# Performance work log

Measured on AMD Instinct MI355X. Metric: run time of the kernel, lower is better.

The kernel has to match this reference:

```python
import jax, jax.numpy as jnp
import numpy as np

D = 512
H = 8
DV = D // H  # 64
NEG_INF = -1e30


def setup_inputs() -> dict:
    key = jax.random.key(0)
    ks = jax.random.split(key, 10)
    B, S = 4, 2048
    x = jax.random.normal(ks[0], (B, D, S), dtype=jnp.float32)
    mask = jnp.ones((B, S), dtype=jnp.float32)
    s = 1.0 / np.sqrt(D)
    sv = 1.0 / np.sqrt(D)
    # per-head Linear(d -> dv) weights stacked: [H, dv, d] (torch Linear layout W @ x)
    Wq = jax.random.uniform(ks[1], (H, DV, D), jnp.float32, -s, s)
    bq = jax.random.uniform(ks[2], (H, DV), jnp.float32, -s, s)
    Wk = jax.random.uniform(ks[3], (H, DV, D), jnp.float32, -s, s)
    bk = jax.random.uniform(ks[4], (H, DV), jnp.float32, -s, s)
    Wv = jax.random.uniform(ks[5], (H, DV, D), jnp.float32, -s, s)
    bv = jax.random.uniform(ks[6], (H, DV), jnp.float32, -s, s)
    W0 = jax.random.uniform(ks[7], (D, D), jnp.float32, -sv, sv)
    b0 = jax.random.uniform(ks[8], (D,), jnp.float32, -sv, sv)
    return {"x": x, "mask": mask, "Wq": Wq, "bq": bq, "Wk": Wk, "bk": bk,
            "Wv": Wv, "bv": bv, "W0": W0, "b0": b0}


def reference(x, mask, Wq, bq, Wk, bk, Wv, bv, W0, b0):
    # x: [B, d, S] -> xt: [B, S, d]
    xt = jnp.transpose(x, (0, 2, 1))
    # fused per-head projections: [B, H, S, dv]
    q = jnp.einsum('bsd,hed->bhse', xt, Wq) + bq[None, :, None, :]
    k = jnp.einsum('bsd,hed->bhse', xt, Wk) + bk[None, :, None, :]
    v = jnp.einsum('bsd,hed->bhse', xt, Wv) + bv[None, :, None, :]
    dv = q.shape[-1]
    scores = jnp.einsum('bhse,bhte->bhst', q, k) * (1.0 / np.sqrt(dv))
    # mask_logits (QANet style): keep where mask==1, else -1e30; mask over key dim
    h_mask = mask[:, None, None, :]  # [B,1,1,S]
    scores = scores * h_mask + (1.0 - h_mask) * NEG_INF
    p = jax.nn.softmax(scores, axis=-1)
    # zero out fully-masked query rows via v_mask on query dim
    p = p * mask[:, None, :, None]
    out = jnp.einsum('bhst,bhte->bhse', p, v)  # [B,H,S,dv]
    # concat heads along feature dim -> [B, S, d]
    B, _, S, _ = out.shape
    heads = jnp.transpose(out, (0, 2, 1, 3)).reshape(B, S, -1)
    y = heads @ W0.T + b0  # output projection
    return jnp.transpose(y, (0, 2, 1))  # [B, d, S]
```

## Files before the change

kernel.cpp:

```cpp
#include <hip/hip_runtime.h>

#define B_  4
#define D_  512
#define H_  8
#define DV_ 64
#define S_  2048
#define LDT 72

typedef __bf16 bf16;
typedef bf16  bf16x8 __attribute__((ext_vector_type(8)));
typedef bf16  bf16x4 __attribute__((ext_vector_type(4)));
typedef float f32x4  __attribute__((ext_vector_type(4)));

#define MFMA(a, b, c) __builtin_amdgcn_mfma_f32_16x16x32_bf16((a), (b), (c), 0, 0, 0)

__global__ __launch_bounds__(256) void transpose_x(const float* __restrict__ x,
                                                   bf16* __restrict__ xb) {
    __shared__ float tile[32][33];
    const int bidx = blockIdx.x;
    const int sblk = bidx % (S_ / 32);
    const int dblk = (bidx / (S_ / 32)) % (D_ / 32);
    const int b    = bidx / ((S_ / 32) * (D_ / 32));
    const int d0 = dblk * 32, s0 = sblk * 32;
    const int tx = threadIdx.x & 31;
    const int ty = threadIdx.x >> 5;
    const float* xp = x + (size_t)b * D_ * S_;
#pragma unroll
    for (int i = 0; i < 32; i += 8)
        tile[ty + i][tx] = xp[(size_t)(d0 + ty + i) * S_ + s0 + tx];
    __syncthreads();
    bf16* xbp = xb + ((size_t)b * S_ + s0) * D_ + d0;
#pragma unroll
    for (int i = 0; i < 32; i += 8)
        xbp[(size_t)(ty + i) * D_ + tx] = (bf16)tile[tx][ty + i];
}

__global__ __launch_bounds__(256) void gemm_qkv(
    const bf16* __restrict__ A,
    const float* __restrict__ Wq, const float* __restrict__ Wk, const float* __restrict__ Wv,
    const float* __restrict__ bq, const float* __restrict__ bk, const float* __restrict__ bv,
    bf16* __restrict__ Q, bf16* __restrict__ K, bf16* __restrict__ Vt) {
    __shared__ bf16 As[128][LDT];
    __shared__ bf16 Bs[64][LDT];

    const int tid  = threadIdx.x;
    const int w    = tid >> 6, lane = tid & 63;
    const int m16  = lane & 15, quad = lane >> 4;

    const int nblk = blockIdx.x % 24;
    const int mblk = blockIdx.x / 24;
    const int m0 = mblk * 128;
    const int n0 = nblk * 64;
    const int proj = n0 >> 9;
    const int nr   = n0 & 511;
    const float* W    = (proj == 0) ? Wq : (proj == 1) ? Wk : Wv;
    const float* bias = (proj == 0) ? bq : (proj == 1) ? bk : bv;

    f32x4 acc[2][4];
#pragma unroll
    for (int i = 0; i < 2; ++i)
#pragma unroll
        for (int j = 0; j < 4; ++j) acc[i][j] = (f32x4){0.f, 0.f, 0.f, 0.f};

    for (int k0 = 0; k0 < D_; k0 += 64) {
        __syncthreads();
        {
            const int col = (tid & 7) * 8;
            const int row = tid >> 3;
#pragma unroll
            for (int p = 0; p < 4; ++p) {
                const int r = row + p * 32;
                *(bf16x8*)&As[r][col] = *(const bf16x8*)&A[(size_t)(m0 + r) * D_ + k0 + col];
            }
        }
        {
            const int col = (tid & 15) * 4;
            const int row = tid >> 4;
#pragma unroll
            for (int p = 0; p < 4; ++p) {
                const int r = row + p * 16;
                const float4 v = *(const float4*)&W[(size_t)(nr + r) * D_ + k0 + col];
                bf16x4 hv = {(bf16)v.x, (bf16)v.y, (bf16)v.z, (bf16)v.w};
                *(bf16x4*)&Bs[r][col] = hv;
            }
        }
        __syncthreads();
#pragma unroll
        for (int kk = 0; kk < 2; ++kk) {
            const bf16x8 a0 = *(const bf16x8*)&As[w * 32 + m16][kk * 32 + quad * 8];
            const bf16x8 a1 = *(const bf16x8*)&As[w * 32 + 16 + m16][kk * 32 + quad * 8];
#pragma unroll
            for (int nt = 0; nt < 4; ++nt) {
                const bf16x8 bfr = *(const bf16x8*)&Bs[nt * 16 + m16][kk * 32 + quad * 8];
                acc[0][nt] = MFMA(a0, bfr, acc[0][nt]);
                acc[1][nt] = MFMA(a1, bfr, acc[1][nt]);
            }
        }
    }

#pragma unroll
    for (int mt = 0; mt < 2; ++mt)
#pragma unroll
        for (int nt = 0; nt < 4; ++nt) {
            const int n = nr + nt * 16 + m16;
            const int h = n >> 6, e = n & 63;
            const float bia = bias[n];
#pragma unroll
            for (int r = 0; r < 4; ++r) {
                const int M = m0 + w * 32 + mt * 16 + quad * 4 + r;
                const int b = M >> 11, s = M & 2047;
                const bf16 hv = (bf16)(acc[mt][nt][r] + bia);
                if (proj == 0)
                    Q[(((size_t)b * H_ + h) * S_ + s) * DV_ + e] = hv;
                else if (proj == 1)
                    K[(((size_t)b * H_ + h) * S_ + s) * DV_ + e] = hv;
                else
                    Vt[(((size_t)b * H_ + h) * DV_ + e) * S_ + s] = hv;
            }
        }
}

__global__ __launch_bounds__(256) void flash_attn(
    const bf16* __restrict__ Q, const bf16* __restrict__ K, const bf16* __restrict__ Vt,
    const float* __restrict__ mask, bf16* __restrict__ heads) {
    __shared__ bf16 Ks[64][LDT];
    __shared__ bf16 Vs[64][LDT];
    __shared__ bf16 Ps[4][16][LDT];
    __shared__ float ms[64];

    const int bidx = blockIdx.x;
    const int qblk = bidx & 31;
    const int h    = (bidx >> 5) & 7;
    const int b    = bidx >> 8;
    const int s0   = qblk * 64;

    const int tid = threadIdx.x;
    const int w = tid >> 6, lane = tid & 63;
    const int m16 = lane & 15, quad = lane >> 4;

    const bf16* Qp = Q + ((size_t)b * H_ + h) * S_ * DV_;
    const bf16* Kp = K + ((size_t)b * H_ + h) * S_ * DV_;
    const bf16* Vp = Vt + ((size_t)b * H_ + h) * DV_ * S_;

    bf16x8 qf[2];
#pragma unroll
    for (int kk = 0; kk < 2; ++kk) {
        bf16x8 v = *(const bf16x8*)&Qp[(size_t)(s0 + w * 16 + m16) * DV_ + kk * 32 + quad * 8];
#pragma unroll
        for (int i = 0; i < 8; ++i) v[i] = (bf16)((float)v[i] * 0.125f);
        qf[kk] = v;
    }

    bf16x8 ones;
#pragma unroll
    for (int i = 0; i < 8; ++i) ones[i] = (bf16)1.0f;

    f32x4 o[4];
    f32x4 lacc = (f32x4){0.f, 0.f, 0.f, 0.f};
#pragma unroll
    for (int et = 0; et < 4; ++et) o[et] = (f32x4){0.f, 0.f, 0.f, 0.f};

    for (int t0 = 0; t0 < S_; t0 += 64) {
        __syncthreads();
        {
            const int col = (tid & 7) * 8;
            const int row = tid >> 3;
#pragma unroll
            for (int p = 0; p < 2; ++p) {
                const int r = row + p * 32;
                *(bf16x8*)&Ks[r][col] = *(const bf16x8*)&Kp[(size_t)(t0 + r) * DV_ + col];
                *(bf16x8*)&Vs[r][col] = *(const bf16x8*)&Vp[(size_t)r * S_ + t0 + col];
            }
            if (tid < 64) ms[tid] = mask[(size_t)b * S_ + t0 + tid];
        }
        __syncthreads();

        f32x4 sc[4];
#pragma unroll
        for (int j = 0; j < 4; ++j) sc[j] = (f32x4){0.f, 0.f, 0.f, 0.f};
#pragma unroll
        for (int kk = 0; kk < 2; ++kk)
#pragma unroll
            for (int nt = 0; nt < 4; ++nt) {
                const bf16x8 bfr = *(const bf16x8*)&Ks[nt * 16 + m16][kk * 32 + quad * 8];
                sc[nt] = MFMA(qf[kk], bfr, sc[nt]);
            }

#pragma unroll
        for (int nt = 0; nt < 4; ++nt) {
            const float mk  = ms[nt * 16 + m16];
            const float neg = (1.0f - mk) * -1e30f;
#pragma unroll
            for (int r = 0; r < 4; ++r) {
                const float p = __expf(sc[nt][r] * mk + neg);
                Ps[w][quad * 4 + r][nt * 16 + m16] = (bf16)p;
            }
        }

#pragma unroll
        for (int kk = 0; kk < 2; ++kk) {
            const bf16x8 pfr = *(const bf16x8*)&Ps[w][m16][kk * 32 + quad * 8];
            lacc = MFMA(ones, pfr, lacc);
#pragma unroll
            for (int et = 0; et < 4; ++et) {
                const bf16x8 vfr = *(const bf16x8*)&Vs[et * 16 + m16][kk * 32 + quad * 8];
                o[et] = MFMA(vfr, pfr, o[et]);
            }
        }
    }

    const int s  = s0 + w * 16 + m16;
    const float qm  = mask[(size_t)b * S_ + s];
    const float inv = qm / lacc[0];
#pragma unroll
    for (int et = 0; et < 4; ++et) {
        bf16x4 hv;
#pragma unroll
        for (int r = 0; r < 4; ++r) hv[r] = (bf16)(o[et][r] * inv);
        *(bf16x4*)&heads[((size_t)b * S_ + s) * D_ + h * DV_ + et * 16 + quad * 4] = hv;
    }
}

__global__ __launch_bounds__(256) void gemm_out(
    const bf16* __restrict__ A, const float* __restrict__ W0,
    const float* __restrict__ b0, float* __restrict__ out) {
    __shared__ bf16 As[128][LDT];
    __shared__ bf16 Bs[64][LDT];

    const int tid = threadIdx.x;
    const int w = tid >> 6, lane = tid & 63;
    const int m16 = lane & 15, quad = lane >> 4;

    const int nblk = blockIdx.x % 8;
    const int mblk = blockIdx.x / 8;
    const int m0 = mblk * 128, n0 = nblk * 64;

    f32x4 acc[2][4];
#pragma unroll
    for (int i = 0; i < 2; ++i)
#pragma unroll
        for (int j = 0; j < 4; ++j) acc[i][j] = (f32x4){0.f, 0.f, 0.f, 0.f};

    for (int k0 = 0; k0 < D_; k0 += 64) {
        __syncthreads();
        {
            const int col = (tid & 7) * 8;
            const int row = tid >> 3;
#pragma unroll
            for (int p = 0; p < 4; ++p) {
                const int r = row + p * 32;
                *(bf16x8*)&As[r][col] = *(const bf16x8*)&A[(size_t)(m0 + r) * D_ + k0 + col];
            }
        }
        {
            const int col = (tid & 15) * 4;
            const int row = tid >> 4;
#pragma unroll
            for (int p = 0; p < 4; ++p) {
                const int r = row + p * 16;
                const float4 v = *(const float4*)&W0[(size_t)(n0 + r) * D_ + k0 + col];
                bf16x4 hv = {(bf16)v.x, (bf16)v.y, (bf16)v.z, (bf16)v.w};
                *(bf16x4*)&Bs[r][col] = hv;
            }
        }
        __syncthreads();
#pragma unroll
        for (int kk = 0; kk < 2; ++kk) {
            const bf16x8 a0 = *(const bf16x8*)&As[w * 32 + m16][kk * 32 + quad * 8];
            const bf16x8 a1 = *(const bf16x8*)&As[w * 32 + 16 + m16][kk * 32 + quad * 8];
#pragma unroll
            for (int nt = 0; nt < 4; ++nt) {
                const bf16x8 bfr = *(const bf16x8*)&Bs[nt * 16 + m16][kk * 32 + quad * 8];
                acc[0][nt] = MFMA(a0, bfr, acc[0][nt]);
                acc[1][nt] = MFMA(a1, bfr, acc[1][nt]);
            }
        }
    }

#pragma unroll
    for (int mt = 0; mt < 2; ++mt)
#pragma unroll
        for (int nt = 0; nt < 4; ++nt) {
            const int n  = n0 + nt * 16 + m16;
            const int Mb = m0 + w * 32 + mt * 16 + quad * 4;
            const int b  = Mb >> 11, s = Mb & 2047;
            const float bia = b0[n];
            float4 vv;
            vv.x = acc[mt][nt][0] + bia;
            vv.y = acc[mt][nt][1] + bia;
            vv.z = acc[mt][nt][2] + bia;
            vv.w = acc[mt][nt][3] + bia;
            *(float4*)&out[((size_t)b * D_ + n) * S_ + s] = vv;
        }
}

extern "C" void kernel_launch(void* const* d_in, const int* in_sizes, int n_in,
                              void* d_out, int out_size, void* d_ws, size_t ws_size,
                              hipStream_t stream) {
    const float* x    = (const float*)d_in[0];
    const float* mask = (const float*)d_in[1];
    const float* Wq   = (const float*)d_in[2];
    const float* bq   = (const float*)d_in[3];
    const float* Wk   = (const float*)d_in[4];
    const float* bk   = (const float*)d_in[5];
    const float* Wv   = (const float*)d_in[6];
    const float* bv   = (const float*)d_in[7];
    const float* W0   = (const float*)d_in[8];
    const float* b0   = (const float*)d_in[9];
    float* out = (float*)d_out;

    char* ws = (char*)d_ws;
    const size_t SEG = (size_t)B_ * S_ * D_ * sizeof(bf16);
    bf16* xb    = (bf16*)(ws);
    bf16* Qb    = (bf16*)(ws + SEG);
    bf16* Kb    = (bf16*)(ws + 2 * SEG);
    bf16* Vt    = (bf16*)(ws + 3 * SEG);
    bf16* heads = xb;

    transpose_x<<<dim3(B_ * (D_ / 32) * (S_ / 32)), dim3(256), 0, stream>>>(x, xb);
    gemm_qkv<<<dim3((B_ * S_ / 128) * (1536 / 64)), dim3(256), 0, stream>>>(
        xb, Wq, Wk, Wv, bq, bk, bv, Qb, Kb, Vt);
    flash_attn<<<dim3(B_ * H_ * (S_ / 64)), dim3(256), 0, stream>>>(Qb, Kb, Vt, mask, heads);
    gemm_out<<<dim3((B_ * S_ / 128) * (D_ / 64)), dim3(256), 0, stream>>>(heads, W0, b0, out);
}
```

Measured before the change: 208.2 us.

## Split attention key range across waves with shared-memory reduction of partial outputs

Restructures flash_attn so each wave owns all 64 query rows but a disjoint 32-key slice of each 128-key step, loading K and V fragments directly from global memory instead of staging them in shared memory. This removes the two block-wide barriers per key tile. The partial O and row-sum accumulators are reduced across waves in shared memory at the end, and the result is written with 16-byte stores. In exchange, register pressure rises (16 O accumulators and 8 Q fragments per lane under a 2-block occupancy bound), each wave reads K/V uncoalesced from global memory, and the final reduction is serialized over four barrier steps.

```diff
diff --git a/kernel.cpp b/kernel.cpp
--- a/kernel.cpp
+++ b/kernel.cpp
@@ -120,105 +120,141 @@
         }
 }
 
-__global__ __launch_bounds__(256) void flash_attn(
+#define RS 36
+__global__ __launch_bounds__(256, 2) void flash_attn(
     const bf16* __restrict__ Q, const bf16* __restrict__ K, const bf16* __restrict__ Vt,
     const float* __restrict__ mask, bf16* __restrict__ heads) {
-    __shared__ bf16 Ks[64][LDT];
-    __shared__ bf16 Vs[64][LDT];
-    __shared__ bf16 Ps[4][16][LDT];
-    __shared__ float ms[64];
+    __shared__ union SMem {
+        bf16 Ps[4][64][RS];
+        struct { float O[64][65]; float L[64]; } red;
+    } sm;
 
     const int bidx = blockIdx.x;
     const int qblk = bidx & 31;
     const int h    = (bidx >> 5) & 7;
     const int b    = bidx >> 8;
-    const int s0   = qblk * 64;
+    const int q0   = qblk * 64;
 
     const int tid = threadIdx.x;
     const int w = tid >> 6, lane = tid & 63;
     const int m16 = lane & 15, quad = lane >> 4;
 
-    const bf16* Qp = Q + ((size_t)b * H_ + h) * S_ * DV_;
-    const bf16* Kp = K + ((size_t)b * H_ + h) * S_ * DV_;
+    const bf16* Qp = Q  + ((size_t)b * H_ + h) * S_ * DV_;
+    const bf16* Kp = K  + ((size_t)b * H_ + h) * S_ * DV_;
     const bf16* Vp = Vt + ((size_t)b * H_ + h) * DV_ * S_;
-
-    bf16x8 qf[2];
-#pragma unroll
-    for (int kk = 0; kk < 2; ++kk) {
-        bf16x8 v = *(const bf16x8*)&Qp[(size_t)(s0 + w * 16 + m16) * DV_ + kk * 32 + quad * 8];
-#pragma unroll
-        for (int i = 0; i < 8; ++i) v[i] = (bf16)((float)v[i] * 0.125f);
-        qf[kk] = v;
+    const float* mp = mask + (size_t)b * S_;
+
+    bf16x8 qf[4][2];
+#pragma unroll
+    for (int mt = 0; mt < 4; ++mt)
+#pragma unroll
+        for (int kk = 0; kk < 2; ++kk) {
+            bf16x8 v = *(const bf16x8*)&Qp[(size_t)(q0 + mt * 16 + m16) * DV_ +
+                                           kk * 32 + quad * 8];
+#pragma unroll
+            for (int i = 0; i < 8; ++i) v[i] = (bf16)((float)v[i] * 0.125f);
+            qf[mt][kk] = v;
+        }
+
+    bf16x8 ones;
+#pragma unroll
+    for (int i = 0; i < 8; ++i) ones[i] = (bf16)1.0f;
+
+    f32x4 o[4][4];
+    f32x4 lacc[4];
+#pragma unroll
+    for (int mt = 0; mt < 4; ++mt)
+#pragma unroll
+        for (int nt = 0; nt < 4; ++nt) o[mt][nt] = (f32x4){0.f, 0.f, 0.f, 0.f};
+#pragma unroll
+    for (int nt = 0; nt < 4; ++nt) lacc[nt] = (f32x4){0.f, 0.f, 0.f, 0.f};
+
+    for (int t0 = 0; t0 < S_; t0 += 128) {
+        const int tw = t0 + w * 32;
+
+        bf16x8 kf[2][2];
+#pragma unroll
+        for (int nt = 0; nt < 2; ++nt)
+#pragma unroll
+            for (int kk = 0; kk < 2; ++kk)
+                kf[nt][kk] = *(const bf16x8*)&Kp[(size_t)(tw + nt * 16 + m16) * DV_ +
+                                                 kk * 32 + quad * 8];
+
+        f32x4 sc[4][2];
+#pragma unroll
+        for (int mt = 0; mt < 4; ++mt)
+#pragma unroll
+            for (int nt = 0; nt < 2; ++nt) sc[mt][nt] = (f32x4){0.f, 0.f, 0.f, 0.f};
+#pragma unroll
+        for (int kk = 0; kk < 2; ++kk)
+#pragma unroll
+            for (int mt = 0; mt < 4; ++mt)
+#pragma unroll
+                for (int nt = 0; nt < 2; ++nt)
+                    sc[mt][nt] = MFMA(qf[mt][kk], kf[nt][kk], sc[mt][nt]);
+
+        const float mk0 = mp[tw + m16],      mk1 = mp[tw + 16 + m16];
+        const float ng0 = (1.0f - mk0) * -1e30f, ng1 = (1.0f - mk1) * -1e30f;
+#pragma unroll
+        for (int mt = 0; mt < 4; ++mt)
+#pragma unroll
+            for (int r = 0; r < 4; ++r) {
+                const int row = mt * 16 + quad * 4 + r;
+                sm.Ps[w][row][m16]      = (bf16)__expf(sc[mt][0][r] * mk0 + ng0);
+                sm.Ps[w][row][16 + m16] = (bf16)__expf(sc[mt][1][r] * mk1 + ng1);
+            }
+
+        bf16x8 pf[4];
+#pragma unroll
+        for (int nt = 0; nt < 4; ++nt)
+            pf[nt] = *(const bf16x8*)&sm.Ps[w][nt * 16 + m16][quad * 8];
+#pragma unroll
+        for (int mt = 0; mt < 4; ++mt) {
+            const bf16x8 vf = *(const bf16x8*)&Vp[(size_t)(mt * 16 + m16) * S_ +
+                                                  tw + quad * 8];
+#pragma unroll
+            for (int nt = 0; nt < 4; ++nt) o[mt][nt] = MFMA(vf, pf[nt], o[mt][nt]);
+        }
+#pragma unroll
+        for (int nt = 0; nt < 4; ++nt) lacc[nt] = MFMA(ones, pf[nt], lacc[nt]);
     }
 
-    bf16x8 ones;
-#pragma unroll
-    for (int i = 0; i < 8; ++i) ones[i] = (bf16)1.0f;
-
-    f32x4 o[4];
-    f32x4 lacc = (f32x4){0.f, 0.f, 0.f, 0.f};
-#pragma unroll
-    for (int et = 0; et < 4; ++et) o[et] = (f32x4){0.f, 0.f, 0.f, 0.f};
-
-    for (int t0 = 0; t0 < S_; t0 += 64) {
-        __syncthreads();
-        {
-            const int col = (tid & 7) * 8;
-            const int row = tid >> 3;
-#pragma unroll
-            for (int p = 0; p < 2; ++p) {
-                const int r = row + p * 32;
-                *(bf16x8*)&Ks[r][col] = *(const bf16x8*)&Kp[(size_t)(t0 + r) * DV_ + col];
-                *(bf16x8*)&Vs[r][col] = *(const bf16x8*)&Vp[(size_t)r * S_ + t0 + col];
-            }
-            if (tid < 64) ms[tid] = mask[(size_t)b * S_ + t0 + tid];
-        }
-        __syncthreads();
-
-        f32x4 sc[4];
-#pragma unroll
-        for (int j = 0; j < 4; ++j) sc[j] = (f32x4){0.f, 0.f, 0.f, 0.f};
-#pragma unroll
-        for (int kk = 0; kk < 2; ++kk)
-#pragma unroll
-            for (int nt = 0; nt < 4; ++nt) {
-                const bf16x8 bfr = *(const bf16x8*)&Ks[nt * 16 + m16][kk * 32 + quad * 8];
-                sc[nt] = MFMA(qf[kk], bfr, sc[nt]);
-            }
-
-#pragma unroll
-        for (int nt = 0; nt < 4; ++nt) {
-            const float mk  = ms[nt * 16 + m16];
-            const float neg = (1.0f - mk) * -1e30f;
-#pragma unroll
-            for (int r = 0; r < 4; ++r) {
-                const float p = __expf(sc[nt][r] * mk + neg);
-                Ps[w][quad * 4 + r][nt * 16 + m16] = (bf16)p;
-            }
-        }
-
-#pragma unroll
-        for (int kk = 0; kk < 2; ++kk) {
-            const bf16x8 pfr = *(const bf16x8*)&Ps[w][m16][kk * 32 + quad * 8];
-            lacc = MFMA(ones, pfr, lacc);
-#pragma unroll
-            for (int et = 0; et < 4; ++et) {
-                const bf16x8 vfr = *(const bf16x8*)&Vs[et * 16 + m16][kk * 32 + quad * 8];
-                o[et] = MFMA(vfr, pfr, o[et]);
-            }
-        }
+    __syncthreads();
+#pragma unroll
+    for (int ww = 0; ww < 4; ++ww) {
+        if (w == ww) {
+#pragma unroll
+            for (int mt = 0; mt < 4; ++mt)
+#pragma unroll
+                for (int nt = 0; nt < 4; ++nt)
+#pragma unroll
+                    for (int r = 0; r < 4; ++r) {
+                        float* slot = &sm.red.O[mt * 16 + quad * 4 + r][nt * 16 + m16];
+                        *slot = (ww == 0) ? o[mt][nt][r] : (*slot + o[mt][nt][r]);
+                    }
+            if (quad == 0)
+#pragma unroll
+                for (int nt = 0; nt < 4; ++nt) {
+                    float* ls = &sm.red.L[nt * 16 + m16];
+                    *ls = (ww == 0) ? lacc[nt][0] : (*ls + lacc[nt][0]);
+                }
+        }
+        __syncthreads();
     }
 
-    const int s  = s0 + w * 16 + m16;
-    const float qm  = mask[(size_t)b * S_ + s];
-    const float inv = qm / lacc[0];
-#pragma unroll
-    for (int et = 0; et < 4; ++et) {
-        bf16x4 hv;
-#pragma unroll
-        for (int r = 0; r < 4; ++r) hv[r] = (bf16)(o[et][r] * inv);
-        *(bf16x4*)&heads[((size_t)b * S_ + s) * D_ + h * DV_ + et * 16 + quad * 4] = hv;
-    }
+    const int ql = tid >> 2, ec = (tid & 3) * 16;
+    const float l  = sm.red.L[ql];
+    const float qm = mp[q0 + ql];
+    const float inv = qm / l;
+    bf16x8 hv[2];
+#pragma unroll
+    for (int c = 0; c < 2; ++c)
+#pragma unroll
+        for (int i = 0; i < 8; ++i)
+            hv[c][i] = (bf16)(sm.red.O[ec + c * 8 + i][ql] * inv);
+    bf16* dst = &heads[((size_t)b * S_ + q0 + ql) * D_ + h * DV_ + ec];
+    *(bf16x8*)(dst)     = hv[0];
+    *(bf16x8*)(dst + 8) = hv[1];
 }
 
 __global__ __launch_bounds__(256) void gemm_out(
```

Result: no change. 208.5 us (+0.2%).
